# Kernel tuning notes

Hardware: AMD Instinct MI355X
Metric: run time of the kernel (lower is better)

The kernel has to match this reference:

```python
import jax, jax.numpy as jnp
import numpy as np

A = 9  # len(scales) * len(ratios) anchor templates
DN = ('NHWC', 'HWIO', 'NHWC')


def _conv(x, w, b):
    y = jax.lax.conv_general_dilated(x, w, window_strides=(1, 1), padding='SAME',
                                     dimension_numbers=DN)
    return y + b


def setup_inputs() -> dict:
    key = jax.random.key(0)
    ks = jax.random.split(key, 9)
    s = 0.02  # weight init scale
    x = jax.random.normal(ks[0], (4, 128, 128, 512), jnp.float32)
    W1 = jax.random.normal(ks[1], (3, 3, 512, 256), jnp.float32) * s
    b1 = jnp.zeros((256,), jnp.float32)
    W2 = jax.random.normal(ks[2], (3, 3, 256, 256), jnp.float32) * s
    b2 = jnp.zeros((256,), jnp.float32)
    Wr = jax.random.normal(ks[3], (1, 1, 256, 4 * A), jnp.float32) * s
    br = jnp.zeros((4 * A,), jnp.float32)
    Wc = jax.random.normal(ks[4], (1, 1, 256, 2 * A), jnp.float32) * s
    bc = jnp.zeros((2 * A,), jnp.float32)
    return {'x': x, 'W1': W1, 'b1': b1, 'W2': W2, 'b2': b2,
            'Wr': Wr, 'br': br, 'Wc': Wc, 'bc': bc}


def reference(x, W1, b1, W2, b2, Wr, br, Wc, bc):
    h = jax.nn.relu(_conv(x, W1, b1))
    h = jax.nn.relu(_conv(h, W2, b2))
    B, H, W = h.shape[0], h.shape[1], h.shape[2]
    reg = _conv(h, Wr, br).reshape(B, H, W, A, 4)            # (B,H,W,A,4)
    cls = _conv(h, Wc, bc).reshape(B, H, W, A, 2)            # (B,H,W,A,2)
    cls = jax.nn.softmax(cls, axis=4)
    return jnp.concatenate((cls, reg), axis=4)               # (B,H,W,A,6)
```

## Files before the change

kernel.cpp:

```cpp
#include <hip/hip_runtime.h>


typedef float f32x4 __attribute__((ext_vector_type(4)));
typedef short bf16x8 __attribute__((ext_vector_type(8)));

union U16x8 { uint4 v; unsigned short s[8]; };

__device__ __forceinline__ unsigned short f2bf(float f) {
  union { float f; unsigned int u; } v; v.f = f;
  unsigned int r = v.u + 0x7FFFu + ((v.u >> 16) & 1u);
  return (unsigned short)(r >> 16);
}

__global__ __launch_bounds__(256) void transpose_cvt(
    const float* __restrict__ src, unsigned short* __restrict__ dst,
    int K, int N) {
  __shared__ float t[32][33];
  const int tx = threadIdx.x, ty = threadIdx.y;
  const int k0 = blockIdx.x * 32, n0 = blockIdx.y * 32;
  const float* s = src + (size_t)blockIdx.z * K * N;
  unsigned short* d = dst + (size_t)blockIdx.z * N * K;
#pragma unroll
  for (int r = 0; r < 32; r += 8) {
    int k = k0 + ty + r, n = n0 + tx;
    t[ty + r][tx] = (k < K && n < N) ? s[(size_t)k * N + n] : 0.f;
  }
  __syncthreads();
#pragma unroll
  for (int r = 0; r < 32; r += 8) {
    int n = n0 + ty + r, k = k0 + tx;
    if (n < N && k < K) d[(size_t)n * K + k] = f2bf(t[tx][ty + r]);
  }
}

__global__ __launch_bounds__(256) void convert_x(
    const float* __restrict__ x, unsigned short* __restrict__ xp) {
  int idx = blockIdx.x * 256 + threadIdx.x;
  int g = idx & 63;
  int cell = idx >> 6;
  int xpix = cell % 130;
  int t = cell / 130;
  int ypix = t % 130;
  int b = t / 130;
  U16x8 u;
  if (xpix == 0 || xpix == 129 || ypix == 0 || ypix == 129) {
    u.v = make_uint4(0u, 0u, 0u, 0u);
  } else {
    const float* sp = x + ((size_t)((b * 128 + ypix - 1) * 128) + (xpix - 1)) * 512 + g * 8;
    float4 a = *(const float4*)sp;
    float4 c = *(const float4*)(sp + 4);
    u.s[0] = f2bf(a.x); u.s[1] = f2bf(a.y); u.s[2] = f2bf(a.z); u.s[3] = f2bf(a.w);
    u.s[4] = f2bf(c.x); u.s[5] = f2bf(c.y); u.s[6] = f2bf(c.z); u.s[7] = f2bf(c.w);
  }
  *(uint4*)(xp + (size_t)cell * 512 + g * 8) = u.v;
}

__global__ __launch_bounds__(256) void zero_h1_borders(unsigned short* __restrict__ h1p) {
  int idx = blockIdx.x * 256 + threadIdx.x;
  int g = idx & 31;
  int cell = idx >> 5;
  int xpix = cell % 130;
  int t = cell / 130;
  int ypix = t % 130;
  if (xpix == 0 || xpix == 129 || ypix == 0 || ypix == 129)
    *(uint4*)(h1p + (size_t)cell * 256 + g * 8) = make_uint4(0u, 0u, 0u, 0u);
}

template<int CIN, int MODE>
__global__ __launch_bounds__(256) void conv3x3(
    const unsigned short* __restrict__ Ap,
    const unsigned short* __restrict__ WT,
    const float* __restrict__ bias,
    unsigned short* __restrict__ out) {
  __shared__ __align__(16) unsigned short As[128][72];
  __shared__ __align__(16) unsigned short Bs[128][72];
  const int tid  = threadIdx.x;
  const int wave = tid >> 6, lane = tid & 63;
  const int wm = wave >> 1, wn = wave & 1;
  const int quad = lane >> 4, l16 = lane & 15;
  const int b = blockIdx.x >> 7, y = blockIdx.x & 127;
  const int nbase = blockIdx.y * 128;

  f32x4 acc[4][4] = {};

  for (int tap = 0; tap < 9; ++tap) {
    const int dy = tap / 3, dx = tap % 3;
    const unsigned short* Abase = Ap + ((size_t)(b * 130 + y + dy) * 130 + dx) * CIN;
    const unsigned short* Bbase = WT + ((size_t)tap * 256 + nbase) * CIN;
    for (int ci0 = 0; ci0 < CIN; ci0 += 64) {
#pragma unroll
      for (int r = 0; r < 4; ++r) {
        int s = r * 256 + tid;
        int row = s >> 3, seg = s & 7;
        uint4 va = *(const uint4*)(Abase + (size_t)row * CIN + ci0 + seg * 8);
        *(uint4*)&As[row][seg * 8] = va;
        uint4 vb = *(const uint4*)(Bbase + (size_t)row * CIN + ci0 + seg * 8);
        *(uint4*)&Bs[row][seg * 8] = vb;
      }
      __syncthreads();
#pragma unroll
      for (int ks = 0; ks < 2; ++ks) {
        bf16x8 af[4], bfr[4];
#pragma unroll
        for (int i = 0; i < 4; ++i)
          af[i] = *(const bf16x8*)&As[wm * 64 + i * 16 + l16][ks * 32 + quad * 8];
#pragma unroll
        for (int j = 0; j < 4; ++j)
          bfr[j] = *(const bf16x8*)&Bs[wn * 64 + j * 16 + l16][ks * 32 + quad * 8];
#pragma unroll
        for (int i = 0; i < 4; ++i)
#pragma unroll
          for (int j = 0; j < 4; ++j)
            acc[i][j] = __builtin_amdgcn_mfma_f32_16x16x32_bf16(af[i], bfr[j], acc[i][j], 0, 0, 0);
      }
      __syncthreads();
    }
  }

#pragma unroll
  for (int i = 0; i < 4; ++i) {
#pragma unroll
    for (int j = 0; j < 4; ++j) {
#pragma unroll
      for (int r = 0; r < 4; ++r) {
        int m = wm * 64 + i * 16 + quad * 4 + r;
        int n = nbase + wn * 64 + j * 16 + l16;
        float v = acc[i][j][r] + bias[n];
        v = fmaxf(v, 0.f);
        size_t off;
        if (MODE == 0)
          off = ((size_t)(b * 130 + y + 1) * 130 + (m + 1)) * 256 + n;
        else
          off = ((size_t)((b * 128 + y) * 128 + m)) * 256 + n;
        out[off] = f2bf(v);
      }
    }
  }
}

__global__ __launch_bounds__(256) void heads_kernel(
    const unsigned short* __restrict__ h2,
    const unsigned short* __restrict__ WhT,
    const float* __restrict__ br, const float* __restrict__ bc,
    float* __restrict__ out) {
  __shared__ __align__(16) unsigned short As[64][264];
  const int tid = threadIdx.x;
  const int wave = tid >> 6, lane = tid & 63;
  const int quad = lane >> 4, l16 = lane & 15;
  const int pix0 = blockIdx.x * 64;
#pragma unroll
  for (int r = 0; r < 8; ++r) {
    int s = r * 256 + tid;
    int row = s >> 5, seg = s & 31;
    *(uint4*)&As[row][seg * 8] =
        *(const uint4*)(h2 + (size_t)(pix0 + row) * 256 + seg * 8);
  }
  __syncthreads();
  f32x4 acc[4] = {};
#pragma unroll
  for (int ks = 0; ks < 8; ++ks) {
    bf16x8 af = *(const bf16x8*)&As[wave * 16 + l16][ks * 32 + quad * 8];
#pragma unroll
    for (int j = 0; j < 4; ++j) {
      bf16x8 bfr = *(const bf16x8*)(WhT + (size_t)(j * 16 + l16) * 256 + ks * 32 + quad * 8);
      acc[j] = __builtin_amdgcn_mfma_f32_16x16x32_bf16(af, bfr, acc[j], 0, 0, 0);
    }
  }
#pragma unroll
  for (int j = 0; j < 4; ++j) {
    int n = j * 16 + l16;
    float bias = 0.f;
    if (n < 18) bias = bc[n];
    else if (n < 54) bias = br[n - 18];
#pragma unroll
    for (int r = 0; r < 4; ++r) {
      int p = pix0 + wave * 16 + quad * 4 + r;
      float v = acc[j][r] + bias;
      float partner = __shfl_xor(v, 1);
      if (n < 18) {
        float mx = fmaxf(v, partner);
        float e0 = __expf(v - mx), e1 = __expf(partner - mx);
        int a = n >> 1, sl = n & 1;
        out[(size_t)p * 54 + a * 6 + sl] = e0 / (e0 + e1);
      } else if (n < 54) {
        int rr = n - 18, a = rr >> 2, sl = (rr & 3) + 2;
        out[(size_t)p * 54 + a * 6 + sl] = v;
      }
    }
  }
}

extern "C" void kernel_launch(void* const* d_in, const int* in_sizes, int n_in,
                              void* d_out, int out_size, void* d_ws, size_t ws_size,
                              hipStream_t stream) {
  const float* x  = (const float*)d_in[0];
  const float* W1 = (const float*)d_in[1];
  const float* b1 = (const float*)d_in[2];
  const float* W2 = (const float*)d_in[3];
  const float* b2 = (const float*)d_in[4];
  const float* Wr = (const float*)d_in[5];
  const float* br = (const float*)d_in[6];
  const float* Wc = (const float*)d_in[7];
  const float* bc = (const float*)d_in[8];
  float* out = (float*)d_out;

  constexpr size_t XPAD_B  = 4ull * 130 * 130 * 512 * 2;
  constexpr size_t H1PAD_B = 4ull * 130 * 130 * 256 * 2;
  constexpr size_t H2_B    = 4ull * 128 * 128 * 256 * 2;
  constexpr size_t W1T_B   = 9ull * 256 * 512 * 2;
  constexpr size_t W2T_B   = 9ull * 256 * 256 * 2;
  char* ws = (char*)d_ws;
  unsigned short* x_pad  = (unsigned short*)(ws);
  unsigned short* h1_pad = (unsigned short*)(ws + XPAD_B);
  unsigned short* h2     = (unsigned short*)(ws + XPAD_B + H1PAD_B);
  unsigned short* W1T    = (unsigned short*)(ws + XPAD_B + H1PAD_B + H2_B);
  unsigned short* W2T    = (unsigned short*)(ws + XPAD_B + H1PAD_B + H2_B + W1T_B);
  unsigned short* WhT    = (unsigned short*)(ws + XPAD_B + H1PAD_B + H2_B + W1T_B + W2T_B);

  hipMemsetAsync(WhT, 0, 64ull * 256 * 2, stream);
  transpose_cvt<<<dim3(16, 8, 9), dim3(32, 8), 0, stream>>>(W1, W1T, 512, 256);
  transpose_cvt<<<dim3(8, 8, 9),  dim3(32, 8), 0, stream>>>(W2, W2T, 256, 256);
  transpose_cvt<<<dim3(8, 1, 1),  dim3(32, 8), 0, stream>>>(Wc, WhT, 256, 18);
  transpose_cvt<<<dim3(8, 2, 1),  dim3(32, 8), 0, stream>>>(Wr, WhT + 18 * 256, 256, 36);
  convert_x<<<16900, 256, 0, stream>>>(x, x_pad);
  zero_h1_borders<<<8450, 256, 0, stream>>>(h1_pad);
  conv3x3<512, 0><<<dim3(512, 2), 256, 0, stream>>>(x_pad, W1T, b1, h1_pad);
  conv3x3<256, 1><<<dim3(512, 2), 256, 0, stream>>>(h1_pad, W2T, b2, h2);
  heads_kernel<<<1024, 256, 0, stream>>>(h2, WhT, br, bc, out);
}
```

Measured before the change: 554.4 us.

## Share one padded input row across three dx taps and use 32x32 MFMA

The conv kernel now loads a 130-pixel padded input row once per dy and reuses it for all three dx taps by offsetting the LDS row index, instead of reloading a 128-row A tile per tap. The weights for the three dx taps are loaded together into a larger LDS buffer. The MFMA switches from 16x16x32 to 32x32x16 with 2x2 f32x16 accumulators, and the epilogue indexing is updated to match. This cuts global A traffic and the number of barriers, at the cost of roughly 1.7x more LDS per block, which may lower occupancy.

```diff
diff --git a/kernel.cpp b/kernel.cpp
--- a/kernel.cpp
+++ b/kernel.cpp
@@ -1,7 +1,8 @@
 #include <hip/hip_runtime.h>
 
 
-typedef float f32x4 __attribute__((ext_vector_type(4)));
+typedef float f32x4  __attribute__((ext_vector_type(4)));
+typedef float f32x16 __attribute__((ext_vector_type(16)));
 typedef short bf16x8 __attribute__((ext_vector_type(8)));
 
 union U16x8 { uint4 v; unsigned short s[8]; };
@@ -72,61 +73,66 @@
     const unsigned short* __restrict__ WT,
     const float* __restrict__ bias,
     unsigned short* __restrict__ out) {
-  __shared__ __align__(16) unsigned short As[128][72];
-  __shared__ __align__(16) unsigned short Bs[128][72];
+  __shared__ __align__(16) unsigned short As[130][72];
+  __shared__ __align__(16) unsigned short Bs[3][128][72];
   const int tid  = threadIdx.x;
   const int wave = tid >> 6, lane = tid & 63;
   const int wm = wave >> 1, wn = wave & 1;
-  const int quad = lane >> 4, l16 = lane & 15;
+  const int l31 = lane & 31, hi = lane >> 5;
   const int b = blockIdx.x >> 7, y = blockIdx.x & 127;
   const int nbase = blockIdx.y * 128;
 
-  f32x4 acc[4][4] = {};
-
-  for (int tap = 0; tap < 9; ++tap) {
-    const int dy = tap / 3, dx = tap % 3;
-    const unsigned short* Abase = Ap + ((size_t)(b * 130 + y + dy) * 130 + dx) * CIN;
-    const unsigned short* Bbase = WT + ((size_t)tap * 256 + nbase) * CIN;
+  f32x16 acc[2][2] = {};
+
+  for (int dy = 0; dy < 3; ++dy) {
+    const unsigned short* Arow = Ap + ((size_t)(b * 130 + y + dy) * 130) * CIN;
+    const unsigned short* Btap = WT + ((size_t)(dy * 3) * 256 + nbase) * CIN;
     for (int ci0 = 0; ci0 < CIN; ci0 += 64) {
-#pragma unroll
-      for (int r = 0; r < 4; ++r) {
-        int s = r * 256 + tid;
+      for (int s = tid; s < 1040; s += 256) {
         int row = s >> 3, seg = s & 7;
-        uint4 va = *(const uint4*)(Abase + (size_t)row * CIN + ci0 + seg * 8);
-        *(uint4*)&As[row][seg * 8] = va;
-        uint4 vb = *(const uint4*)(Bbase + (size_t)row * CIN + ci0 + seg * 8);
-        *(uint4*)&Bs[row][seg * 8] = vb;
+        *(uint4*)&As[row][seg * 8] =
+            *(const uint4*)(Arow + (size_t)row * CIN + ci0 + seg * 8);
+      }
+#pragma unroll
+      for (int t = 0; t < 12; ++t) {
+        int s = t * 256 + tid;
+        int dx = s >> 10, r = (s >> 3) & 127, seg = s & 7;
+        *(uint4*)&Bs[dx][r][seg * 8] =
+            *(const uint4*)(Btap + ((size_t)dx * 256 + r) * CIN + ci0 + seg * 8);
       }
       __syncthreads();
 #pragma unroll
-      for (int ks = 0; ks < 2; ++ks) {
-        bf16x8 af[4], bfr[4];
-#pragma unroll
-        for (int i = 0; i < 4; ++i)
-          af[i] = *(const bf16x8*)&As[wm * 64 + i * 16 + l16][ks * 32 + quad * 8];
-#pragma unroll
-        for (int j = 0; j < 4; ++j)
-          bfr[j] = *(const bf16x8*)&Bs[wn * 64 + j * 16 + l16][ks * 32 + quad * 8];
-#pragma unroll
-        for (int i = 0; i < 4; ++i)
-#pragma unroll
-          for (int j = 0; j < 4; ++j)
-            acc[i][j] = __builtin_amdgcn_mfma_f32_16x16x32_bf16(af[i], bfr[j], acc[i][j], 0, 0, 0);
+      for (int dx = 0; dx < 3; ++dx) {
+#pragma unroll
+        for (int ks = 0; ks < 4; ++ks) {
+          bf16x8 af[2], bfr[2];
+#pragma unroll
+          for (int i = 0; i < 2; ++i)
+            af[i] = *(const bf16x8*)&As[wm * 64 + i * 32 + l31 + dx][ks * 16 + hi * 8];
+#pragma unroll
+          for (int j = 0; j < 2; ++j)
+            bfr[j] = *(const bf16x8*)&Bs[dx][wn * 64 + j * 32 + l31][ks * 16 + hi * 8];
+#pragma unroll
+          for (int i = 0; i < 2; ++i)
+#pragma unroll
+            for (int j = 0; j < 2; ++j)
+              acc[i][j] = __builtin_amdgcn_mfma_f32_32x32x16_bf16(af[i], bfr[j], acc[i][j], 0, 0, 0);
+        }
       }
       __syncthreads();
     }
   }
 
 #pragma unroll
-  for (int i = 0; i < 4; ++i) {
-#pragma unroll
-    for (int j = 0; j < 4; ++j) {
-#pragma unroll
-      for (int r = 0; r < 4; ++r) {
-        int m = wm * 64 + i * 16 + quad * 4 + r;
-        int n = nbase + wn * 64 + j * 16 + l16;
-        float v = acc[i][j][r] + bias[n];
-        v = fmaxf(v, 0.f);
+  for (int i = 0; i < 2; ++i) {
+#pragma unroll
+    for (int j = 0; j < 2; ++j) {
+      int n = nbase + wn * 64 + j * 32 + l31;
+      float bb = bias[n];
+#pragma unroll
+      for (int reg = 0; reg < 16; ++reg) {
+        int m = wm * 64 + i * 32 + (reg & 3) + 8 * (reg >> 2) + 4 * hi;
+        float v = fmaxf(acc[i][j][reg] + bb, 0.f);
         size_t off;
         if (MODE == 0)
           off = ((size_t)(b * 130 + y + 1) * 130 + (m + 1)) * 256 + n;
```

Result: faster. 511.7 us (-7.7%).
